# Optimization experiments

Measured on AMD Instinct MI355X. Metric: run time of the kernel, lower is better.

## Reference

```python
import jax, jax.numpy as jnp
import numpy as np

B, N, I, H = 4, 325, 64, 128
LN_EPS = 1e-5

def setup_inputs() -> dict:
    key = jax.random.key(0)
    ks = jax.random.split(key, 20)
    x = jax.random.normal(ks[0], (B, N, I), dtype=jnp.float32)
    # sparse binary adjacency with self-loops (as the module masks adj == 0)
    a = (jax.random.uniform(ks[1], (B, N, N)) < 0.05).astype(jnp.float32)
    adj = jnp.maximum(a, jnp.eye(N, dtype=jnp.float32)[None])
    h = jax.random.normal(ks[2], (B, N, H), dtype=jnp.float32)
    c = jax.random.normal(ks[3], (B, N, H), dtype=jnp.float32)
    def glorot(k, shape):
        fan_in, fan_out = shape[-1], shape[0]
        s = jnp.sqrt(2.0 / (fan_in + fan_out)).astype(jnp.float32)
        return jax.random.normal(k, shape, dtype=jnp.float32) * s
    params = {
        'W_ih': glorot(ks[4], (4 * H, I)),
        'W_hh': glorot(ks[5], (4 * H, H)),
        'b_ih': jnp.zeros((4 * H,), jnp.float32),
        'b_hh': jnp.zeros((4 * H,), jnp.float32),
        'gc_w': glorot(ks[6], (H, H)),
        'gc_b': jnp.zeros((H,), jnp.float32),
        'Ws_w': glorot(ks[7], (H, H)),
        'Ws_b': jnp.zeros((H,), jnp.float32),
        'Wt_w': glorot(ks[8], (H, H)),
        'Wt_b': jnp.zeros((H,), jnp.float32),
        'v': glorot(ks[9], (H, 1)),
        'ln_g': jnp.ones((H,), jnp.float32),
        'ln_b': jnp.zeros((H,), jnp.float32),
        'comb_w': glorot(ks[10], (H, 2 * H)),
        'comb_b': jnp.zeros((H,), jnp.float32),
    }
    return {'x': x, 'adj': adj, 'h': h, 'c': c, **params}


def reference(x, adj, h, c, W_ih, W_hh, b_ih, b_hh, gc_w, gc_b,
              Ws_w, Ws_b, Wt_w, Wt_b, v, ln_g, ln_b, comb_w, comb_b):
    # --- LSTMCell applied per node (PyTorch gate order: i, f, g, o) ---
    gates = (jnp.einsum('bni,gi->bng', x, W_ih) + b_ih
             + jnp.einsum('bnh,gh->bng', h, W_hh) + b_hh)  # [B,N,4H]
    i_g, f_g, g_g, o_g = jnp.split(gates, 4, axis=-1)
    c_lstm = jax.nn.sigmoid(f_g) * c + jax.nn.sigmoid(i_g) * jnp.tanh(g_g)
    h_lstm = jax.nn.sigmoid(o_g) * jnp.tanh(c_lstm)  # [B,N,H]
    # --- Graph convolution: adj @ (h W) + b ---
    support = jnp.einsum('bnh,ho->bno', h_lstm, gc_w)
    h_graph = jnp.einsum('bnm,bmo->bno', adj, support) + gc_b
    # --- Spatial attention (tanh-additive, adjacency-masked softmax) ---
    s = jnp.einsum('bnh,oh->bno', h_graph, Ws_w) + Ws_b  # W_s(x)
    t = jnp.einsum('bnh,oh->bno', h_graph, Wt_w) + Wt_b  # W_t(x)
    # scores[b,i,j] = tanh(s[b,i] + t[b,j]) @ v ; big [B,N,N,H] intermediate
    scores = jnp.einsum('bijh,h->bij',
                        jnp.tanh(s[:, :, None, :] + t[:, None, :, :]),
                        v[:, 0])
    scores = jnp.where(adj == 0, -1e9, scores)
    attn = jax.nn.softmax(scores, axis=-1)
    context = jnp.einsum('bij,bjh->bih', attn, h_graph)
    # --- LayerNorm ---
    mu = jnp.mean(context, axis=-1, keepdims=True)
    var = jnp.var(context, axis=-1, keepdims=True)
    h_att = ln_g * (context - mu) * jax.lax.rsqrt(var + LN_EPS) + ln_b
    # --- Combine ---
    h_comb = jnp.concatenate([h_lstm, h_att], axis=-1)
    h_new = jnp.einsum('bnk,ok->bno', h_comb, comb_w) + comb_b
    return (h_new, c_lstm)
```

## Files before the change

kernel.cpp:

```cpp
#include <hip/hip_runtime.h>

#define B_ 4
#define N_ 325
#define I_ 64
#define H_ 128
#define NODES (B_ * N_)
#define NZMAX 64
#define NBLK (NODES / 4)

typedef unsigned short u16;
typedef unsigned int u32;

__device__ __align__(16) float g_WT   [192 * 512];
__device__ __align__(16) float g_gcw  [128 * 128];
__device__ __align__(16) float g_WsT  [128 * 128];
__device__ __align__(16) float g_WtT  [128 * 128];
__device__ __align__(16) float g_combT[256 * 128];
__device__ float g_bias[512];
__device__ float g_svec[896];

__device__ __align__(16) float g_support[(size_t)NODES * H_];
__device__ __align__(16) float g_h_graph[(size_t)NODES * H_];
__device__ __align__(16) float g_t_buf  [(size_t)NODES * H_];
__device__ __align__(16) float g_s_buf  [(size_t)NODES * H_];
__device__ __align__(16) float g_hl     [(size_t)NODES * H_];
__device__ u16   g_nz [(size_t)NODES * NZMAX];
__device__ float g_nzw[(size_t)NODES * NZMAX];
__device__ int   g_nzc[NODES];

__device__ __forceinline__ float bf2f(u16 u) { return __uint_as_float(((u32)u) << 16); }
__device__ __forceinline__ u16 f2bf(float f) {
    u32 u = __float_as_uint(f);
    u += 0x7fffu + ((u >> 16) & 1u);
    return (u16)(u >> 16);
}
__device__ __forceinline__ float ldin(const void* p, size_t i, int f32) {
    return f32 ? ((const float*)p)[i] : bf2f(((const u16*)p)[i]);
}
__device__ __forceinline__ void stout(void* p, size_t i, float v, int f32) {
    if (f32) ((float*)p)[i] = v; else ((u16*)p)[i] = f2bf(v);
}
__device__ __forceinline__ float fast_rcp(float x) { return __builtin_amdgcn_rcpf(x); }
__device__ __forceinline__ float sigm(float x) { return fast_rcp(1.f + __expf(-x)); }
__device__ __forceinline__ float tanh_f(float x) {
    x = fminf(15.f, fmaxf(-15.f, x));
    float e = __expf(2.f * x);
    return (e - 1.f) * fast_rcp(e + 1.f);
}
__device__ __forceinline__ int probe_f32(const void* adj) {
    return ((((const u32*)adj)[0] & 0xFFFFu) != 0x3F80u) ? 1 : 0;
}

__global__ __launch_bounds__(256) void k0_prep(
    const void* __restrict__ W_ih, const void* __restrict__ W_hh,
    const void* __restrict__ b_ih, const void* __restrict__ b_hh,
    const void* __restrict__ gc_w, const void* __restrict__ gc_b,
    const void* __restrict__ Ws_w, const void* __restrict__ Ws_b,
    const void* __restrict__ Wt_w, const void* __restrict__ Wt_b,
    const void* __restrict__ vvec, const void* __restrict__ ln_g,
    const void* __restrict__ ln_b, const void* __restrict__ comb_w,
    const void* __restrict__ comb_b, const void* __restrict__ adj)
{
    const int f32 = probe_f32(adj);
    const int tid = blockIdx.x * 256 + threadIdx.x;
    const int nth = gridDim.x * 256;
    const int TOT = 98304 + 16384 * 3 + 32768 + 512 + 896;
    for (int e = tid; e < TOT; e += nth) {
        int i = e;
        if (i < 98304) {
            const int k = i >> 9, g = i & 511;
            g_WT[i] = (k < 64) ? ldin(W_ih, (size_t)g * 64 + k, f32)
                               : ldin(W_hh, (size_t)g * 128 + (k - 64), f32);
            continue;
        }
        i -= 98304;
        if (i < 16384) { g_gcw[i] = ldin(gc_w, i, f32); continue; }
        i -= 16384;
        if (i < 16384) {
            const int k = i >> 7, o = i & 127;
            g_WsT[i] = ldin(Ws_w, (size_t)o * 128 + k, f32);
            continue;
        }
        i -= 16384;
        if (i < 16384) {
            const int k = i >> 7, o = i & 127;
            g_WtT[i] = ldin(Wt_w, (size_t)o * 128 + k, f32);
            continue;
        }
        i -= 16384;
        if (i < 32768) {
            const int k = i >> 7, o = i & 127;
            g_combT[i] = ldin(comb_w, (size_t)o * 256 + k, f32);
            continue;
        }
        i -= 32768;
        if (i < 512) { g_bias[i] = ldin(b_ih, i, f32) + ldin(b_hh, i, f32); continue; }
        i -= 512;
        {
            const int seg = i >> 7, k = i & 127;
            const void* src = (seg == 0) ? gc_b : (seg == 1) ? Ws_b : (seg == 2) ? Wt_b :
                              (seg == 3) ? vvec : (seg == 4) ? ln_g : (seg == 5) ? ln_b : comb_b;
            g_svec[i] = ldin(src, k, f32);
        }
    }
}

__global__ __launch_bounds__(512) void k1_lstm(
    const void* __restrict__ x, const void* __restrict__ h, const void* __restrict__ c,
    const void* __restrict__ adj, void* __restrict__ out)
{
    const int f32 = probe_f32(adj);
    __shared__ __align__(16) float4 xh4[192];
    __shared__ __align__(16) float4 Gt4[512];
    __shared__ __align__(16) float4 hl4[128];
    __shared__ u16 nzi[4][NZMAX];
    __shared__ float nzv[4][NZMAX];
    __shared__ int cnt[4];
    const int node0 = blockIdx.x * 4;
    const int t = threadIdx.x;

    if (t < 4) cnt[t] = 0;
    for (int e = t; e < 768; e += 512) {
        const int n = e / 192, k = e % 192;
        const int node = node0 + n;
        ((float*)&xh4[k])[n] = (k < 64) ? ldin(x, (size_t)node * 64 + k, f32)
                                        : ldin(h, (size_t)node * 128 + (k - 64), f32);
    }
    __syncthreads();

    {
        const int g = t;
        float a0 = 0.f, a1 = 0.f, a2 = 0.f, a3 = 0.f;
        #pragma unroll 8
        for (int k = 0; k < 192; ++k) {
            const float wv = g_WT[(size_t)k * 512 + g];
            const float4 xv = xh4[k];
            a0 = fmaf(xv.x, wv, a0); a1 = fmaf(xv.y, wv, a1);
            a2 = fmaf(xv.z, wv, a2); a3 = fmaf(xv.w, wv, a3);
        }
        const float bias = g_bias[g];
        Gt4[g] = make_float4(a0 + bias, a1 + bias, a2 + bias, a3 + bias);
    }
    __syncthreads();

    {
        const int n = t >> 7, hh = t & 127;
        const int node = node0 + n;
        float ig = ((const float*)&Gt4[hh])[n];
        float fg = ((const float*)&Gt4[128 + hh])[n];
        float gv = ((const float*)&Gt4[256 + hh])[n];
        float og = ((const float*)&Gt4[384 + hh])[n];
        float cl = sigm(fg) * ldin(c, (size_t)node * 128 + hh, f32) + sigm(ig) * tanh_f(gv);
        float hv = sigm(og) * tanh_f(cl);
        stout(out, (size_t)(NODES * H_) + (size_t)node * 128 + hh, cl, f32);
        g_hl[(size_t)node * 128 + hh] = hv;
        ((float*)&hl4[hh])[n] = hv;
    }
    {
        const int n = t >> 7, jj = t & 127;
        const size_t row = (size_t)(node0 + n) * N_;
        for (int j = jj; j < N_; j += 128) {
            float a = ldin(adj, row + j, f32);
            if (a != 0.f) {
                int p = atomicAdd(&cnt[n], 1);
                if (p < NZMAX) { nzi[n][p] = (u16)j; nzv[n][p] = a; }
            }
        }
    }
    __syncthreads();

    if (t < 4) g_nzc[node0 + t] = min(cnt[t], NZMAX);
    #pragma unroll
    for (int n = 0; n < 4; ++n) {
        const int cnn = min(cnt[n], NZMAX);
        for (int p = t; p < cnn; p += 512) {
            g_nz [(size_t)(node0 + n) * NZMAX + p] = nzi[n][p];
            g_nzw[(size_t)(node0 + n) * NZMAX + p] = nzv[n][p];
        }
    }
    {
        const int o = t & 127, n = t >> 7;
        float acc = 0.f;
        #pragma unroll 8
        for (int k = 0; k < 128; ++k)
            acc = fmaf(((const float*)&hl4[k])[n], g_gcw[(size_t)k * 128 + o], acc);
        g_support[(size_t)(node0 + n) * 128 + o] = acc;
    }
}

__global__ __launch_bounds__(512) void k2_graph(const void* __restrict__ adj)
{
    (void)adj;
    __shared__ __align__(16) float4 hg4[128];
    __shared__ u16 nzi[4][NZMAX];
    __shared__ float nzv[4][NZMAX];
    __shared__ int cnt[4];
    __shared__ float part[4][4][H_];
    const int node0 = blockIdx.x * 4;
    const int t = threadIdx.x;

    if (t < 4) cnt[t] = g_nzc[node0 + t];
    __syncthreads();
    #pragma unroll
    for (int n = 0; n < 4; ++n) {
        const int cnn = cnt[n];
        for (int p = t; p < cnn; p += 512) {
            nzi[n][p] = g_nz [(size_t)(node0 + n) * NZMAX + p];
            nzv[n][p] = g_nzw[(size_t)(node0 + n) * NZMAX + p];
        }
    }
    __syncthreads();

    {
        const int n = t >> 7, o = t & 127;
        const int node = node0 + n;
        const int bn = node / N_;
        const int cnn = cnt[n];
        float acc = g_svec[o];
        for (int p = 0; p < cnn; ++p)
            acc = fmaf(nzv[n][p], g_support[((size_t)bn * N_ + nzi[n][p]) * 128 + o], acc);
        g_h_graph[(size_t)node * 128 + o] = acc;
        ((float*)&hg4[o])[n] = acc;
    }
    __syncthreads();

    {
        const int o = t & 127;
        const int which = (t >> 7) & 1;
        const int half  = t >> 8;
        const float* WT = which ? g_WtT : g_WsT;
        const int k0 = half * 64;
        float a0 = 0.f, a1 = 0.f, a2 = 0.f, a3 = 0.f;
        #pragma unroll 8
        for (int kk = 0; kk < 64; ++kk) {
            const int k = k0 + kk;
            const float wv = WT[(size_t)k * 128 + o];
            const float4 hv = hg4[k];
            a0 = fmaf(hv.x, wv, a0); a1 = fmaf(hv.y, wv, a1);
            a2 = fmaf(hv.z, wv, a2); a3 = fmaf(hv.w, wv, a3);
        }
        const int s = which * 2 + half;
        part[s][0][o] = a0; part[s][1][o] = a1;
        part[s][2][o] = a2; part[s][3][o] = a3;
    }
    __syncthreads();
    for (int e = t; e < 1024; e += 512) {
        const int which = e >> 9, n = (e >> 7) & 3, o = e & 127;
        const float vsum = part[which * 2][n][o] + part[which * 2 + 1][n][o]
                         + g_svec[128 + which * 128 + o];
        float* dst = which ? g_t_buf : g_s_buf;
        dst[(size_t)(node0 + n) * 128 + o] = vsum;
    }
}

__global__ __launch_bounds__(512) void k3_attn(
    const void* __restrict__ adj, void* __restrict__ out)
{
    const int f32 = probe_f32(adj);
    __shared__ __align__(16) float4 hl4[128];
    __shared__ __align__(16) float4 att4[128];
    __shared__ float s_i[4][H_];
    __shared__ float red[4][H_];
    __shared__ float nzs[4][NZMAX];
    __shared__ u16 nzi[4][NZMAX];
    __shared__ float part[4][4][H_];
    __shared__ float mu_[4], rstd_[4], smv[4];
    __shared__ int cnt[4];
    const int node0 = blockIdx.x * 4;
    const int t = threadIdx.x;
    const int lane = t & 63, w = t >> 6;

    if (t < 4) cnt[t] = g_nzc[node0 + t];
    for (int e = t; e < 512; e += 512) {
        const int n = e >> 7, k = e & 127;
        const int node = node0 + n;
        s_i[n][k] = g_s_buf[(size_t)node * 128 + k];
        ((float*)&hl4[k])[n] = g_hl[(size_t)node * 128 + k];
    }
    __syncthreads();
    #pragma unroll
    for (int n = 0; n < 4; ++n)
        for (int p = t; p < cnt[n]; p += 512)
            nzi[n][p] = g_nz[(size_t)(node0 + n) * NZMAX + p];
    __syncthreads();

    {
        const int n = w & 3;
        const int bn = (node0 + n) / N_;
        const int cn = cnt[n];
        const float v0 = g_svec[384 + lane], v1 = g_svec[384 + 64 + lane];
        const float si0 = s_i[n][lane], si1 = s_i[n][lane + 64];
        for (int p = (w >> 2); p < cn; p += 2) {
            const float* tj = g_t_buf + ((size_t)bn * N_ + nzi[n][p]) * 128;
            float a = v0 * tanh_f(si0 + tj[lane]) + v1 * tanh_f(si1 + tj[lane + 64]);
            #pragma unroll
            for (int off = 32; off > 0; off >>= 1) a += __shfl_xor(a, off);
            if (lane == 0) nzs[n][p] = a;
        }
    }
    __syncthreads();
    if (t < 4) {
        const int cn = cnt[t];
        float m = -1e30f;
        for (int p = 0; p < cn; ++p) m = fmaxf(m, nzs[t][p]);
        float ssum = 0.f;
        for (int p = 0; p < cn; ++p) { float e = __expf(nzs[t][p] - m); nzs[t][p] = e; ssum += e; }
        smv[t] = fast_rcp(ssum);
    }
    __syncthreads();

    {
        const int n = t >> 7, o = t & 127;
        const int bn = (node0 + n) / N_;
        const int cn = cnt[n];
        float acc = 0.f;
        for (int p = 0; p < cn; ++p)
            acc = fmaf(nzs[n][p], g_h_graph[((size_t)bn * N_ + nzi[n][p]) * 128 + o], acc);
        red[n][o] = acc * smv[n];
    }
    __syncthreads();

    if (w < 4) {
        float x0 = red[w][lane], x1 = red[w][lane + 64];
        float sm = x0 + x1, sq = x0 * x0 + x1 * x1;
        #pragma unroll
        for (int off = 32; off > 0; off >>= 1) {
            sm += __shfl_xor(sm, off);
            sq += __shfl_xor(sq, off);
        }
        if (lane == 0) {
            float mu = sm * (1.f / H_);
            float var = fmaxf(sq * (1.f / H_) - mu * mu, 0.f);
            mu_[w] = mu;
            rstd_[w] = __builtin_amdgcn_rsqf(var + 1e-5f);
        }
    }
    __syncthreads();
    {
        const int n = t >> 7, k = t & 127;
        float xn = (red[n][k] - mu_[n]) * rstd_[n];
        ((float*)&att4[k])[n] = g_svec[512 + k] * xn + g_svec[640 + k];
    }
    __syncthreads();

    {
        const int o = t & 127, q = t >> 7;
        const float4* src = (q < 2) ? hl4 : att4;
        const int kb = (q < 2) ? q * 64 : (q - 2) * 64;
        const int k0 = q * 64;
        float a0 = 0.f, a1 = 0.f, a2 = 0.f, a3 = 0.f;
        #pragma unroll 8
        for (int kk = 0; kk < 64; ++kk) {
            const float wv = g_combT[(size_t)(k0 + kk) * 128 + o];
            const float4 cv = src[kb + kk];
            a0 = fmaf(cv.x, wv, a0); a1 = fmaf(cv.y, wv, a1);
            a2 = fmaf(cv.z, wv, a2); a3 = fmaf(cv.w, wv, a3);
        }
        part[q][0][o] = a0; part[q][1][o] = a1;
        part[q][2][o] = a2; part[q][3][o] = a3;
    }
    __syncthreads();
    {
        const int n = t >> 7, k = t & 127;
        stout(out, (size_t)(node0 + n) * 128 + k,
              part[0][n][k] + part[1][n][k] + part[2][n][k] + part[3][n][k]
              + g_svec[768 + k], f32);
    }
}

extern "C" void kernel_launch(void* const* d_in, const int* in_sizes, int n_in,
                              void* d_out, int out_size, void* d_ws, size_t ws_size,
                              hipStream_t stream)
{
    (void)in_sizes; (void)n_in; (void)out_size; (void)d_ws; (void)ws_size;
    const void* x      = d_in[0];
    const void* adj    = d_in[1];
    const void* h      = d_in[2];
    const void* c      = d_in[3];
    const void* W_ih   = d_in[4];
    const void* W_hh   = d_in[5];
    const void* b_ih   = d_in[6];
    const void* b_hh   = d_in[7];
    const void* gc_w   = d_in[8];
    const void* gc_b   = d_in[9];
    const void* Ws_w   = d_in[10];
    const void* Ws_b   = d_in[11];
    const void* Wt_w   = d_in[12];
    const void* Wt_b   = d_in[13];
    const void* vvec   = d_in[14];
    const void* ln_g   = d_in[15];
    const void* ln_b   = d_in[16];
    const void* comb_w = d_in[17];
    const void* comb_b = d_in[18];

    k0_prep <<<256, 256, 0, stream>>>(W_ih, W_hh, b_ih, b_hh, gc_w, gc_b,
                                      Ws_w, Ws_b, Wt_w, Wt_b, vvec, ln_g, ln_b,
                                      comb_w, comb_b, adj);
    k1_lstm <<<NBLK, 512, 0, stream>>>(x, h, c, adj, d_out);
    k2_graph<<<NBLK, 512, 0, stream>>>(adj);
    k3_attn <<<NBLK, 512, 0, stream>>>(adj, d_out);
}
```

Before: 141.1 us.

## Flatten attention score work into a task list with 16-lane groups; coalesce weight-transpose writes

The attention score phase now builds a compact shared-memory list of (node, neighbor) tasks across the four nodes in a block. Each 16-lane subgroup handles one task, with 8 dimensions per lane and a 4-step shuffle reduction, replacing one full wavefront per neighbor with a 6-step reduction. This aims to raise lane utilization and balance work when neighbor counts differ between nodes. The prep kernel's transposes now iterate in source order (coalesced reads, strided writes), and the redundant loop around the s_i/hl load is removed.

```diff
diff --git a/kernel.cpp b/kernel.cpp
--- a/kernel.cpp
+++ b/kernel.cpp
@@ -68,29 +68,30 @@
     for (int e = tid; e < TOT; e += nth) {
         int i = e;
         if (i < 98304) {
-            const int k = i >> 9, g = i & 511;
-            g_WT[i] = (k < 64) ? ldin(W_ih, (size_t)g * 64 + k, f32)
-                               : ldin(W_hh, (size_t)g * 128 + (k - 64), f32);
+            const int g = i / 192, kk = i % 192;
+            const float v = (kk < 64) ? ldin(W_ih, (size_t)g * 64 + kk, f32)
+                                      : ldin(W_hh, (size_t)g * 128 + (kk - 64), f32);
+            g_WT[(size_t)kk * 512 + g] = v;
             continue;
         }
         i -= 98304;
         if (i < 16384) { g_gcw[i] = ldin(gc_w, i, f32); continue; }
         i -= 16384;
         if (i < 16384) {
-            const int k = i >> 7, o = i & 127;
-            g_WsT[i] = ldin(Ws_w, (size_t)o * 128 + k, f32);
+            const int o = i >> 7, k = i & 127;
+            g_WsT[(size_t)k * 128 + o] = ldin(Ws_w, (size_t)o * 128 + k, f32);
             continue;
         }
         i -= 16384;
         if (i < 16384) {
-            const int k = i >> 7, o = i & 127;
-            g_WtT[i] = ldin(Wt_w, (size_t)o * 128 + k, f32);
+            const int o = i >> 7, k = i & 127;
+            g_WtT[(size_t)k * 128 + o] = ldin(Wt_w, (size_t)o * 128 + k, f32);
             continue;
         }
         i -= 16384;
         if (i < 32768) {
-            const int k = i >> 7, o = i & 127;
-            g_combT[i] = ldin(comb_w, (size_t)o * 256 + k, f32);
+            const int o = i >> 8, k = i & 255;
+            g_combT[(size_t)k * 128 + o] = ldin(comb_w, (size_t)o * 256 + k, f32);
             continue;
         }
         i -= 32768;
@@ -263,6 +264,7 @@
     __shared__ float red[4][H_];
     __shared__ float nzs[4][NZMAX];
     __shared__ u16 nzi[4][NZMAX];
+    __shared__ u16 tasks[4 * NZMAX];
     __shared__ float part[4][4][H_];
     __shared__ float mu_[4], rstd_[4], smv[4];
     __shared__ int cnt[4];
@@ -271,8 +273,8 @@
     const int lane = t & 63, w = t >> 6;
 
     if (t < 4) cnt[t] = g_nzc[node0 + t];
-    for (int e = t; e < 512; e += 512) {
-        const int n = e >> 7, k = e & 127;
+    {
+        const int n = t >> 7, k = t & 127;
         const int node = node0 + n;
         s_i[n][k] = g_s_buf[(size_t)node * 128 + k];
         ((float*)&hl4[k])[n] = g_hl[(size_t)node * 128 + k];
@@ -282,20 +284,37 @@
     for (int n = 0; n < 4; ++n)
         for (int p = t; p < cnt[n]; p += 512)
             nzi[n][p] = g_nz[(size_t)(node0 + n) * NZMAX + p];
-    __syncthreads();
-
-    {
-        const int n = w & 3;
-        const int bn = (node0 + n) / N_;
-        const int cn = cnt[n];
-        const float v0 = g_svec[384 + lane], v1 = g_svec[384 + 64 + lane];
-        const float si0 = s_i[n][lane], si1 = s_i[n][lane + 64];
-        for (int p = (w >> 2); p < cn; p += 2) {
+    if (t < 256) {
+        const int n = t >> 6, p = t & 63;
+        if (p < cnt[n]) {
+            int base = 0;
+            #pragma unroll
+            for (int m = 0; m < 3; ++m) base += (m < n) ? cnt[m] : 0;
+            tasks[base + p] = (u16)t;
+        }
+    }
+    __syncthreads();
+
+    {
+        const int grp = lane >> 4, d0 = lane & 15;
+        const int TT = cnt[0] + cnt[1] + cnt[2] + cnt[3];
+        float vreg[8];
+        #pragma unroll
+        for (int r = 0; r < 8; ++r) vreg[r] = g_svec[384 + d0 + 16 * r];
+        for (int it = w * 4 + grp; it < TT; it += 32) {
+            const int s = tasks[it];
+            const int n = s >> 6, p = s & 63;
+            const int bn = (node0 + n) / N_;
             const float* tj = g_t_buf + ((size_t)bn * N_ + nzi[n][p]) * 128;
-            float a = v0 * tanh_f(si0 + tj[lane]) + v1 * tanh_f(si1 + tj[lane + 64]);
+            float a = 0.f;
             #pragma unroll
-            for (int off = 32; off > 0; off >>= 1) a += __shfl_xor(a, off);
-            if (lane == 0) nzs[n][p] = a;
+            for (int r = 0; r < 8; ++r) {
+                const int d = d0 + 16 * r;
+                a = fmaf(vreg[r], tanh_f(s_i[n][d] + tj[d]), a);
+            }
+            #pragma unroll
+            for (int off = 8; off > 0; off >>= 1) a += __shfl_xor(a, off);
+            if (d0 == 0) nzs[n][p] = a;
         }
     }
     __syncthreads();
```

Result: faster. 134.0 us (median of 2 runs) (-5.1%).
